# Kernel optimization log

Hardware: AMD Instinct MI355X
Metric: run time of the kernel (lower is better)

Reference implementation:

```python
import jax, jax.numpy as jnp
import numpy as np
from jax import lax

B, J, C, K, TOK, CH, H = 2048, 17, 480, 3, 64, 960, 6
HD = C // H  # 80
EPS = 1e-5

def gelu(x):
    return jax.nn.gelu(x, approximate=False)

def layernorm(x, g, b):
    mu = jnp.mean(x, axis=-1, keepdims=True)
    var = jnp.var(x, axis=-1, keepdims=True)
    return (x - mu) * lax.rsqrt(var + EPS) * g + b

def groupnorm(x, g, b, groups=16):
    # x: (B, C, J) -> normalize over (C//groups * J) per group
    n, c, j = x.shape
    xg = x.reshape(n, groups, -1)
    mu = jnp.mean(xg, axis=-1, keepdims=True)
    var = jnp.var(xg, axis=-1, keepdims=True)
    xg = (xg - mu) * lax.rsqrt(var + EPS)
    return xg.reshape(n, c, j) * g[None, :, None] + b[None, :, None]

def dwconv1d(x, w, b, pad):
    # x: (B, C, J), w: (C, 1, Kw) depthwise
    y = lax.conv_general_dilated(x, w, window_strides=(1,), padding=[(pad, pad)],
                                 dimension_numbers=('NCH', 'OIH', 'NCH'),
                                 feature_group_count=x.shape[1])
    return y + b[None, :, None]

def setup_inputs() -> dict:
    key = jax.random.key(0)
    ks = jax.random.split(key, 16)
    n = jax.random.normal
    return {
        'x': n(ks[0], (B, J, C), dtype=jnp.float32),
        'adj': n(ks[1], (K, J, J), dtype=jnp.float32) * 0.1,
        'norm1_g': jnp.ones((J,), jnp.float32), 'norm1_b': jnp.zeros((J,), jnp.float32),
        'gcn1_w': n(ks[2], (C * K, C), jnp.float32) * 0.02, 'gcn1_b': jnp.zeros((C * K,), jnp.float32),
        'dw_w': n(ks[3], (C, 1, 7), jnp.float32) * 0.1, 'dw_b': jnp.zeros((C,), jnp.float32),
        'dwgn_g': jnp.ones((C,), jnp.float32), 'dwgn_b': jnp.zeros((C,), jnp.float32),
        'mlp1_w1': n(ks[4], (TOK, J), jnp.float32) * 0.02, 'mlp1_b1': jnp.zeros((TOK,), jnp.float32),
        'mlp1_w2': n(ks[5], (J, TOK), jnp.float32) * 0.02, 'mlp1_b2': jnp.zeros((J,), jnp.float32),
        'qkv_w': n(ks[6], (3 * C, C), jnp.float32) * 0.02, 'qkv_b': jnp.zeros((3 * C,), jnp.float32),
        'proj_w': n(ks[7], (C, C), jnp.float32) * 0.02, 'proj_b': jnp.zeros((C,), jnp.float32),
        'pos_w': n(ks[8], (C, 1, 9), jnp.float32) * 0.1, 'pos_b': jnp.zeros((C,), jnp.float32),
        'gnf_g': jnp.ones((C,), jnp.float32), 'gnf_b': jnp.zeros((C,), jnp.float32),
        'norm2_g': jnp.ones((C,), jnp.float32), 'norm2_b': jnp.zeros((C,), jnp.float32),
        'gcn2_w': n(ks[9], (C * K, C), jnp.float32) * 0.02, 'gcn2_b': jnp.zeros((C * K,), jnp.float32),
        'mlp2_w1': n(ks[10], (CH, C), jnp.float32) * 0.02, 'mlp2_b1': jnp.zeros((CH,), jnp.float32),
        'mlp2_w2': n(ks[11], (C, CH), jnp.float32) * 0.02, 'mlp2_b2': jnp.zeros((C,), jnp.float32),
    }

def reference(x, adj, norm1_g, norm1_b, gcn1_w, gcn1_b, dw_w, dw_b, dwgn_g, dwgn_b,
              mlp1_w1, mlp1_b1, mlp1_w2, mlp1_b2, qkv_w, qkv_b, proj_w, proj_b,
              pos_w, pos_b, gnf_g, gnf_b, norm2_g, norm2_b, gcn2_w, gcn2_b,
              mlp2_w1, mlp2_b1, mlp2_w2, mlp2_b2):
    b = x.shape[0]
    xc = jnp.transpose(x, (0, 2, 1))            # (b, c, j)
    res_spatial = xc
    xn = layernorm(xc, norm1_g, norm1_b)        # LN over joints
    # --- GCN branch 1: 1x1 conv then adjacency einsum ---
    y = jnp.einsum('bcj,oc->boj', xn, gcn1_w) + gcn1_b[None, :, None]
    y = y.reshape(b, K, C, J)
    x_gcn1 = jnp.einsum('bkcv,kvw->bcw', y, adj)  # (b, c, j)
    # --- depthwise conv + GN + GELU + token Mlp ---
    d = gelu(groupnorm(dwconv1d(xn, dw_w, dw_b, 3), dwgn_g, dwgn_b))
    x_mjem = gelu(d @ mlp1_w1.T + mlp1_b1) @ mlp1_w2.T + mlp1_b2  # mix over j
    # --- spatial global attention (6 heads over joints + dwconv pos) ---
    xt = jnp.transpose(xn, (0, 2, 1))           # (b, j, c)
    qkv = xt @ qkv_w.T + qkv_b                  # (b, j, 3c)
    qkv = qkv.reshape(b, J, 3, H, HD).transpose(2, 0, 3, 1, 4)  # (3, b, h, j, hd)
    q, k, v = qkv[0], qkv[1], qkv[2]
    attn = jax.nn.softmax(jnp.einsum('bhqd,bhkd->bhqk', q, k) * (HD ** -0.5), axis=-1)
    o = jnp.einsum('bhqk,bhkd->bhqd', attn, v).transpose(0, 2, 1, 3).reshape(b, J, C)
    o = o @ proj_w.T + proj_b
    x_gsa = jnp.transpose(o, (0, 2, 1)) + dwconv1d(xn, pos_w, pos_b, 4)  # (b, c, j)
    # --- fuse ---
    fused = groupnorm(x_gsa + x_gcn1 + x_mjem, gnf_g, gnf_b)
    xc = res_spatial + gelu(fused)
    # --- channel stage ---
    xj = jnp.transpose(xc, (0, 2, 1))           # (b, j, c)
    res_channel = xj
    xn2 = layernorm(xj, norm2_g, norm2_b)       # LN over channels
    xcc = jnp.transpose(xn2, (0, 2, 1))         # (b, c, j)
    y2 = jnp.einsum('bcj,oc->boj', xcc, gcn2_w) + gcn2_b[None, :, None]
    y2 = y2.reshape(b, K, C, J)
    x_gcn2 = jnp.transpose(jnp.einsum('bkcv,kvw->bcw', y2, adj), (0, 2, 1))  # (b, j, c)
    mlp_out = gelu(xn2 @ mlp2_w1.T + mlp2_b1) @ mlp2_w2.T + mlp2_b2
    # sca_block is undefined in the source __init__ -> identity
    return res_channel + mlp_out + x_gcn2
```

## Files before the change

kernel.cpp:

```cpp
#include <hip/hip_runtime.h>
#include <hip/hip_bf16.h>

#define DI __device__ __forceinline__

typedef __attribute__((ext_vector_type(8))) short bf16x8;
typedef __attribute__((ext_vector_type(4))) float f32x4;

namespace {
constexpr int B_ = 2048, J_ = 17, C_ = 480, K_ = 3, TOK_ = 64, CH_ = 960, H_ = 6, HD_ = 80;
constexpr int C3_ = 3 * C_;
constexpr float EPSF = 1e-5f;
}

DI float gelu_f(float x) { return 0.5f * x * (1.0f + erff(x * 0.70710678118654752f)); }
DI float b2f(__hip_bfloat16 v) { return __bfloat162float(v); }
DI __hip_bfloat16 f2b(float v) { return __float2bfloat16(v); }
DI float s2f(short s) { return __uint_as_float(((unsigned)(unsigned short)s) << 16); }

DI void gl16(const void* g, void* l) {
  __builtin_amdgcn_global_load_lds(
      (const __attribute__((address_space(1))) unsigned int*)g,
      (__attribute__((address_space(3))) unsigned int*)l, 16, 0, 0);
}

__global__ __launch_bounds__(256) void cvt_all_kernel(
    const float* __restrict__ s0, const float* __restrict__ s1,
    const float* __restrict__ s2, const float* __restrict__ s3,
    const float* __restrict__ s4, const float* __restrict__ s5,
    __hip_bfloat16* __restrict__ d) {
  constexpr int SG = C3_ * C_;
  constexpr int O1 = SG, O2 = 2 * SG, O3 = 3 * SG;
  constexpr int O4 = O3 + C_ * C_;
  constexpr int O5 = O4 + CH_ * C_;
  const int i = (blockIdx.x * 256 + threadIdx.x) * 4;
  const float* s; int off;
  if      (i < O1) { s = s0; off = i; }
  else if (i < O2) { s = s1; off = i - O1; }
  else if (i < O3) { s = s2; off = i - O2; }
  else if (i < O4) { s = s3; off = i - O3; }
  else if (i < O5) { s = s4; off = i - O4; }
  else             { s = s5; off = i - O5; }
  const float4 v = *reinterpret_cast<const float4*>(s + off);
  union { ushort4 u; __hip_bfloat16 h[4]; } o;
  o.h[0] = f2b(v.x); o.h[1] = f2b(v.y); o.h[2] = f2b(v.z); o.h[3] = f2b(v.w);
  *reinterpret_cast<ushort4*>(reinterpret_cast<unsigned short*>(d) + i) = o.u;
}

__global__ __launch_bounds__(256) void ln1_kernel(const float* __restrict__ x,
                                                  const float* __restrict__ g,
                                                  const float* __restrict__ bt,
                                                  __hip_bfloat16* __restrict__ xnT, int nBC) {
  const int t = blockIdx.x * 256 + threadIdx.x;
  if (t >= nBC) return;
  const int b = t / C_, c = t % C_;
  const float* xp = x + (size_t)b * J_ * C_ + c;
  float v[J_];
  float s = 0.f;
  #pragma unroll
  for (int j = 0; j < J_; ++j) { v[j] = xp[j * C_]; s += v[j]; }
  const float mu = s * (1.f / J_);
  float sq = 0.f;
  #pragma unroll
  for (int j = 0; j < J_; ++j) { const float d = v[j] - mu; sq += d * d; }
  const float rs = rsqrtf(sq * (1.f / J_) + EPSF);
  __hip_bfloat16* op = xnT + (size_t)b * J_ * C_ + c;
  #pragma unroll
  for (int j = 0; j < J_; ++j) op[j * C_] = f2b((v[j] - mu) * rs * g[j] + bt[j]);
}

template<int KD, int EPI>
__global__ __launch_bounds__(256) void gemm_lds(const __hip_bfloat16* __restrict__ A,
                                                const __hip_bfloat16* __restrict__ W,
                                                const float* __restrict__ bias,
                                                __hip_bfloat16* __restrict__ Dst, int Ntot,
                                                const __hip_bfloat16* __restrict__ r1,
                                                const __hip_bfloat16* __restrict__ r2,
                                                float* __restrict__ outf) {
  constexpr int NST = (KD + 63) / 64;
  constexpr bool TAIL = (KD % 64) != 0;
  constexpr int ROWB = KD * 2;
  __shared__ __align__(16) char smem[57344];

  const int lane = threadIdx.x & 63;
  const int wid  = threadIdx.x >> 6;
  const int m0g = blockIdx.x * 128;
  const int n0g = blockIdx.y * 96;

  const int srow = lane >> 3;
  const int scbs = ((lane & 7) * 16) ^ ((srow & 7) << 4);
  auto stage = [&](int t, int bi) {
    const int kb = t * 128;
    const int ab = bi * 16384;
    const int bb = 32768 + bi * 12288;
    #pragma unroll
    for (int i = wid; i < 16; i += 4) {
      const int r = i * 8 + srow;
      gl16((const char*)A + (size_t)(m0g + r) * ROWB + kb + scbs, smem + ab + i * 1024);
    }
    #pragma unroll
    for (int i = wid; i < 12; i += 4) {
      const int r = i * 8 + srow;
      gl16((const char*)W + (size_t)(n0g + r) * ROWB + kb + scbs, smem + bb + i * 1024);
    }
  };

  const f32x4 zf = {0.f, 0.f, 0.f, 0.f};
  f32x4 acc[4][3];
  #pragma unroll
  for (int mi = 0; mi < 4; ++mi)
    #pragma unroll
    for (int ni = 0; ni < 3; ++ni) acc[mi][ni] = zf;

  const int rA0 = (wid >> 1) * 64 + (lane & 15);
  const int rB0 = (wid & 1) * 48 + (lane & 15);
  const int swz = (lane & 7) << 4;
  const int kq  = (lane >> 4) * 16;

  stage(0, 0);
  __syncthreads();
  int buf = 0;
  for (int t = 0; t < NST; ++t) {
    if (t + 1 < NST) stage(t + 1, buf ^ 1);
    const int abase = buf * 16384;
    const int bbase = 32768 + buf * 12288;
    const int nks = (TAIL && t == NST - 1) ? 1 : 2;
    for (int ks = 0; ks < nks; ++ks) {
      const int cb = (ks * 64 + kq) ^ swz;
      bf16x8 av[4], bv[3];
      #pragma unroll
      for (int mi = 0; mi < 4; ++mi)
        av[mi] = *reinterpret_cast<const bf16x8*>(smem + abase + (rA0 + mi * 16) * 128 + cb);
      #pragma unroll
      for (int ni = 0; ni < 3; ++ni)
        bv[ni] = *reinterpret_cast<const bf16x8*>(smem + bbase + (rB0 + ni * 16) * 128 + cb);
      #pragma unroll
      for (int mi = 0; mi < 4; ++mi)
        #pragma unroll
        for (int ni = 0; ni < 3; ++ni)
          acc[mi][ni] = __builtin_amdgcn_mfma_f32_16x16x32_bf16(av[mi], bv[ni], acc[mi][ni], 0, 0, 0);
    }
    __syncthreads();
    buf ^= 1;
  }

  const int col0 = n0g + (wid & 1) * 48 + (lane & 15);
  const int r0   = m0g + (wid >> 1) * 64 + ((lane >> 4) << 2);
  #pragma unroll
  for (int ni = 0; ni < 3; ++ni) {
    const int col = col0 + ni * 16;
    const float bvv = bias[col];
    #pragma unroll
    for (int mi = 0; mi < 4; ++mi) {
      #pragma unroll
      for (int r = 0; r < 4; ++r) {
        const size_t idx = (size_t)(r0 + mi * 16 + r) * Ntot + col;
        float v = acc[mi][ni][r] + bvv;
        if (EPI == 1) v = gelu_f(v);
        if (EPI == 2) outf[idx] = v + b2f(r1[idx]) + b2f(r2[idx]);
        else Dst[idx] = f2b(v);
      }
    }
  }
}

__global__ __launch_bounds__(256) void attn_kernel(const __hip_bfloat16* __restrict__ qkv,
                                                   __hip_bfloat16* __restrict__ o) {
  const int b = blockIdx.x, tid = threadIdx.x;
  __shared__ __hip_bfloat16 sqkv[J_][C3_];
  __shared__ float S[H_][J_][J_];
  {
    const uint4* src = (const uint4*)(qkv + (size_t)b * J_ * C3_);
    uint4* dst = (uint4*)&sqkv[0][0];
    for (int i = tid; i < 3060; i += 256) dst[i] = src[i];
  }
  __syncthreads();
  for (int i = tid; i < H_ * J_ * J_; i += 256) {
    const int h = i / (J_ * J_), r = i % (J_ * J_), qj = r / J_, kj = r % J_;
    const bf16x8* qp = (const bf16x8*)&sqkv[qj][h * HD_];
    const bf16x8* kp = (const bf16x8*)&sqkv[kj][C_ + h * HD_];
    float acc = 0.f;
    #pragma unroll
    for (int d8 = 0; d8 < HD_ / 8; ++d8) {
      const bf16x8 qv = qp[d8], kv = kp[d8];
      #pragma unroll
      for (int t = 0; t < 8; ++t) acc += s2f(qv[t]) * s2f(kv[t]);
    }
    S[h][qj][kj] = acc * 0.11180339887498949f;
  }
  __syncthreads();
  if (tid < H_ * J_) {
    const int h = tid / J_, qj = tid % J_;
    float* row = S[h][qj];
    float m = row[0];
    #pragma unroll
    for (int kk = 1; kk < J_; ++kk) m = fmaxf(m, row[kk]);
    float s = 0.f;
    #pragma unroll
    for (int kk = 0; kk < J_; ++kk) { const float e = __expf(row[kk] - m); row[kk] = e; s += e; }
    const float inv = 1.f / s;
    #pragma unroll
    for (int kk = 0; kk < J_; ++kk) row[kk] *= inv;
  }
  __syncthreads();
  __hip_bfloat16* ob = o + (size_t)b * J_ * C_;
  for (int i = tid; i < J_ * C_; i += 256) {
    const int qj = i / C_, c = i % C_;
    const int h = c / HD_;
    const float* srow = S[h][qj];
    float acc = 0.f;
    #pragma unroll
    for (int kk = 0; kk < J_; ++kk) acc += srow[kk] * b2f(sqkv[kk][2 * C_ + c]);
    ob[i] = f2b(acc);
  }
}

__global__ __launch_bounds__(512) void gcn_contract_kernel(const __hip_bfloat16* __restrict__ y,
                                                           const float* __restrict__ adj,
                                                           __hip_bfloat16* __restrict__ g) {
  const int b = blockIdx.x, tid = threadIdx.x;
  __shared__ float adjl[K_ * J_ * J_];
  for (int i = tid; i < K_ * J_ * J_; i += 512) adjl[i] = adj[i];
  __syncthreads();
  const int c = tid;
  if (c < C_) {
    float yv[K_][J_];
    const __hip_bfloat16* yb = y + (size_t)b * J_ * C3_ + c;
    #pragma unroll
    for (int k = 0; k < K_; ++k)
      #pragma unroll
      for (int v = 0; v < J_; ++v)
        yv[k][v] = b2f(yb[(size_t)v * C3_ + k * C_]);
    __hip_bfloat16* gp = g + (size_t)b * J_ * C_ + c;
    #pragma unroll
    for (int w = 0; w < J_; ++w) {
      float acc = 0.f;
      #pragma unroll
      for (int k = 0; k < K_; ++k)
        #pragma unroll
        for (int v = 0; v < J_; ++v)
          acc += yv[k][v] * adjl[(k * J_ + v) * J_ + w];
      gp[w * C_] = f2b(acc);
    }
  }
}

__global__ __launch_bounds__(512) void dwmlp_kernel(const __hip_bfloat16* __restrict__ xnT,
    const float* __restrict__ dww, const float* __restrict__ dwb,
    const float* __restrict__ gg, const float* __restrict__ gb,
    const float* __restrict__ w1, const float* __restrict__ b1,
    const float* __restrict__ w2, const float* __restrict__ b2,
    __hip_bfloat16* __restrict__ mjem) {
  const int b = blockIdx.x, tid = threadIdx.x;
  __shared__ __hip_bfloat16 xl[J_][C_];
  __shared__ float gstat[16][2];
  {
    const uint4* src = (const uint4*)(xnT + (size_t)b * J_ * C_);
    uint4* dst = (uint4*)&xl[0][0];
    for (int i = tid; i < 1020; i += 512) dst[i] = src[i];
  }
  if (tid < 32) gstat[tid >> 1][tid & 1] = 0.f;
  __syncthreads();
  const int c = tid;
  float dv[J_];
  if (c < C_) {
    float wv[7];
    #pragma unroll
    for (int t = 0; t < 7; ++t) wv[t] = dww[c * 7 + t];
    const float bias = dwb[c];
    float s = 0.f, sqs = 0.f;
    #pragma unroll
    for (int j = 0; j < J_; ++j) {
      float acc = bias;
      #pragma unroll
      for (int t = 0; t < 7; ++t) {
        const int jj = j - 3 + t;
        if (jj >= 0 && jj < J_) acc += b2f(xl[jj][c]) * wv[t];
      }
      dv[j] = acc; s += acc; sqs += acc * acc;
    }
    atomicAdd(&gstat[c / 30][0], s);
    atomicAdd(&gstat[c / 30][1], sqs);
  }
  __syncthreads();
  if (c < C_) {
    const float mu = gstat[c / 30][0] * (1.f / 510.f);
    const float var = gstat[c / 30][1] * (1.f / 510.f) - mu * mu;
    const float rs = rsqrtf(var + EPSF);
    const float sc = gg[c], of = gb[c];
    #pragma unroll
    for (int j = 0; j < J_; ++j) dv[j] = gelu_f((dv[j] - mu) * rs * sc + of);
    float h[TOK_];
    #pragma unroll
    for (int t = 0; t < TOK_; ++t) h[t] = b1[t];
    #pragma unroll
    for (int j = 0; j < J_; ++j) {
      const float d = dv[j];
      #pragma unroll
      for (int t = 0; t < TOK_; ++t) h[t] = fmaf(d, w1[t * J_ + j], h[t]);
    }
    #pragma unroll
    for (int t = 0; t < TOK_; ++t) h[t] = gelu_f(h[t]);
    float mj[J_];
    #pragma unroll
    for (int j = 0; j < J_; ++j) mj[j] = b2[j];
    #pragma unroll
    for (int t = 0; t < TOK_; ++t) {
      const float hg = h[t];
      #pragma unroll
      for (int j = 0; j < J_; ++j) mj[j] = fmaf(hg, w2[j * TOK_ + t], mj[j]);
    }
    __hip_bfloat16* dst = mjem + (size_t)b * J_ * C_ + c;
    #pragma unroll
    for (int j = 0; j < J_; ++j) dst[j * C_] = f2b(mj[j]);
  }
}

__global__ __launch_bounds__(512) void fuse_kernel(
    const float* __restrict__ x, const __hip_bfloat16* __restrict__ xnT,
    const __hip_bfloat16* __restrict__ g1o, const __hip_bfloat16* __restrict__ projo,
    const __hip_bfloat16* __restrict__ mjem,
    const float* __restrict__ posw, const float* __restrict__ posb,
    const float* __restrict__ gnfg, const float* __restrict__ gnfb,
    const float* __restrict__ n2g, const float* __restrict__ n2b,
    __hip_bfloat16* __restrict__ resch, __hip_bfloat16* __restrict__ xn2) {
  const int b = blockIdx.x, tid = threadIdx.x;
  __shared__ float xcl[J_][C_];
  __shared__ float gstat[16][2];
  __shared__ float lnst[J_][2];
  if (tid < 32) gstat[tid >> 1][tid & 1] = 0.f;
  __syncthreads();
  const int c = tid;
  float fz[J_];
  if (c < C_) {
    float xnv[J_];
    const __hip_bfloat16* xp = xnT + (size_t)b * J_ * C_ + c;
    #pragma unroll
    for (int j = 0; j < J_; ++j) xnv[j] = b2f(xp[j * C_]);
    float pw[9];
    #pragma unroll
    for (int t = 0; t < 9; ++t) pw[t] = posw[c * 9 + t];
    const float pb = posb[c];
    const __hip_bfloat16* pj = projo + (size_t)b * J_ * C_ + c;
    const __hip_bfloat16* mp = mjem + (size_t)b * J_ * C_ + c;
    const __hip_bfloat16* gp = g1o + (size_t)b * J_ * C_ + c;
    float s = 0.f, sqs = 0.f;
    #pragma unroll
    for (int j = 0; j < J_; ++j) {
      float pos = pb;
      #pragma unroll
      for (int t = 0; t < 9; ++t) {
        const int jj = j - 4 + t;
        if (jj >= 0 && jj < J_) pos += xnv[jj] * pw[t];
      }
      const float f = b2f(pj[j * C_]) + pos + b2f(gp[j * C_]) + b2f(mp[j * C_]);
      fz[j] = f; s += f; sqs += f * f;
    }
    atomicAdd(&gstat[c / 30][0], s);
    atomicAdd(&gstat[c / 30][1], sqs);
  }
  __syncthreads();
  if (c < C_) {
    const float mu = gstat[c / 30][0] * (1.f / 510.f);
    const float var = gstat[c / 30][1] * (1.f / 510.f) - mu * mu;
    const float rs = rsqrtf(var + EPSF);
    const float sc = gnfg[c], of = gnfb[c];
    const float* xr = x + (size_t)b * J_ * C_ + c;
    __hip_bfloat16* rp = resch + (size_t)b * J_ * C_ + c;
    #pragma unroll
    for (int j = 0; j < J_; ++j) {
      const float xcv = xr[j * C_] + gelu_f((fz[j] - mu) * rs * sc + of);
      xcl[j][c] = xcv;
      rp[j * C_] = f2b(xcv);
    }
  }
  __syncthreads();
  const int wid = tid >> 6, lane = tid & 63;
  for (int j = wid; j < J_; j += 8) {
    float ls = 0.f, lq = 0.f;
    for (int cc = lane; cc < C_; cc += 64) { const float v = xcl[j][cc]; ls += v; lq += v * v; }
    #pragma unroll
    for (int off = 32; off > 0; off >>= 1) { ls += __shfl_xor(ls, off); lq += __shfl_xor(lq, off); }
    if (lane == 0) {
      const float mu = ls * (1.f / C_);
      const float var = lq * (1.f / C_) - mu * mu;
      lnst[j][0] = mu; lnst[j][1] = rsqrtf(var + EPSF);
    }
  }
  __syncthreads();
  if (c < C_) {
    const float sc = n2g[c], of = n2b[c];
    __hip_bfloat16* xp2 = xn2 + (size_t)b * J_ * C_ + c;
    #pragma unroll
    for (int j = 0; j < J_; ++j)
      xp2[j * C_] = f2b((xcl[j][c] - lnst[j][0]) * lnst[j][1] * sc + of);
  }
}

extern "C" void kernel_launch(void* const* d_in, const int* in_sizes, int n_in,
                              void* d_out, int out_size, void* d_ws, size_t ws_size,
                              hipStream_t stream) {
  const float* x      = (const float*)d_in[0];
  const float* adj    = (const float*)d_in[1];
  const float* n1g    = (const float*)d_in[2];
  const float* n1b    = (const float*)d_in[3];
  const float* gcn1_w = (const float*)d_in[4];
  const float* gcn1_b = (const float*)d_in[5];
  const float* dw_w   = (const float*)d_in[6];
  const float* dw_b   = (const float*)d_in[7];
  const float* dwgn_g = (const float*)d_in[8];
  const float* dwgn_b = (const float*)d_in[9];
  const float* m1w1   = (const float*)d_in[10];
  const float* m1b1   = (const float*)d_in[11];
  const float* m1w2   = (const float*)d_in[12];
  const float* m1b2   = (const float*)d_in[13];
  const float* qkv_w  = (const float*)d_in[14];
  const float* qkv_b  = (const float*)d_in[15];
  const float* proj_w = (const float*)d_in[16];
  const float* proj_b = (const float*)d_in[17];
  const float* pos_w  = (const float*)d_in[18];
  const float* pos_b  = (const float*)d_in[19];
  const float* gnf_g  = (const float*)d_in[20];
  const float* gnf_b  = (const float*)d_in[21];
  const float* n2g    = (const float*)d_in[22];
  const float* n2b    = (const float*)d_in[23];
  const float* gcn2_w = (const float*)d_in[24];
  const float* gcn2_b = (const float*)d_in[25];
  const float* m2w1   = (const float*)d_in[26];
  const float* m2b1   = (const float*)d_in[27];
  const float* m2w2   = (const float*)d_in[28];
  const float* m2b2   = (const float*)d_in[29];
  float* out = (float*)d_out;
  char* ws = (char*)d_ws;
  (void)in_sizes; (void)n_in; (void)out_size;

  auto a256 = [](size_t b) { return (b + 255) & ~(size_t)255; };
  const size_t wbytes = 3 * a256((size_t)C3_ * C_ * 2) + a256((size_t)C_ * C_ * 2) +
                        a256((size_t)CH_ * C_ * 2) + a256((size_t)C_ * CH_ * 2);
  int nch = 16;
  for (int cand : {1, 2, 4, 8, 16}) {
    const size_t Mcb = (size_t)(B_ / cand) * J_;
    const size_t fp = wbytes + a256(Mcb * C3_ * 2) + 6 * a256(Mcb * C_ * 2);
    if (fp <= ws_size) { nch = cand; break; }
  }
  const int Bc = B_ / nch;
  const int Mc = Bc * J_;

  size_t off = 0;
  auto alloc = [&](size_t bytes) { char* p = ws + off; off += a256(bytes); return p; };
  __hip_bfloat16* w_qkv = (__hip_bfloat16*)alloc((size_t)C3_ * C_ * 2);
  __hip_bfloat16* w_g1  = (__hip_bfloat16*)alloc((size_t)C3_ * C_ * 2);
  __hip_bfloat16* w_g2  = (__hip_bfloat16*)alloc((size_t)C3_ * C_ * 2);
  __hip_bfloat16* w_pr  = (__hip_bfloat16*)alloc((size_t)C_ * C_ * 2);
  __hip_bfloat16* w_21  = (__hip_bfloat16*)alloc((size_t)CH_ * C_ * 2);
  __hip_bfloat16* w_22  = (__hip_bfloat16*)alloc((size_t)C_ * CH_ * 2);
  __hip_bfloat16* BIG   = (__hip_bfloat16*)alloc((size_t)Mc * C3_ * 2);
  __hip_bfloat16* xnT   = (__hip_bfloat16*)alloc((size_t)Mc * C_ * 2);
  __hip_bfloat16* attno = (__hip_bfloat16*)alloc((size_t)Mc * C_ * 2);
  __hip_bfloat16* projo = (__hip_bfloat16*)alloc((size_t)Mc * C_ * 2);
  __hip_bfloat16* mjem  = (__hip_bfloat16*)alloc((size_t)Mc * C_ * 2);
  __hip_bfloat16* g1o   = (__hip_bfloat16*)alloc((size_t)Mc * C_ * 2);
  __hip_bfloat16* resch = (__hip_bfloat16*)alloc((size_t)Mc * C_ * 2);
  __hip_bfloat16* xn2   = attno;
  __hip_bfloat16* g2o   = g1o;
  __hip_bfloat16* hbuf  = BIG;

  cvt_all_kernel<<<3150, 256, 0, stream>>>(qkv_w, gcn1_w, gcn2_w, proj_w, m2w1, m2w2, w_qkv);

  for (int ci = 0; ci < nch; ++ci) {
    const float* xc = x + (size_t)ci * Bc * J_ * C_;
    float* outc = out + (size_t)ci * Bc * J_ * C_;
    ln1_kernel<<<(Bc * C_ + 255) / 256, 256, 0, stream>>>(xc, n1g, n1b, xnT, Bc * C_);
    gemm_lds<C_, 0><<<dim3(Mc / 128, C3_ / 96), 256, 0, stream>>>(xnT, w_qkv, qkv_b, BIG, C3_, nullptr, nullptr, nullptr);
    attn_kernel<<<Bc, 256, 0, stream>>>(BIG, attno);
    gemm_lds<C_, 0><<<dim3(Mc / 128, C3_ / 96), 256, 0, stream>>>(xnT, w_g1, gcn1_b, BIG, C3_, nullptr, nullptr, nullptr);
    gcn_contract_kernel<<<Bc, 512, 0, stream>>>(BIG, adj, g1o);
    gemm_lds<C_, 0><<<dim3(Mc / 128, C_ / 96), 256, 0, stream>>>(attno, w_pr, proj_b, projo, C_, nullptr, nullptr, nullptr);
    dwmlp_kernel<<<Bc, 512, 0, stream>>>(xnT, dw_w, dw_b, dwgn_g, dwgn_b, m1w1, m1b1, m1w2, m1b2, mjem);
    fuse_kernel<<<Bc, 512, 0, stream>>>(xc, xnT, g1o, projo, mjem, pos_w, pos_b,
                                        gnf_g, gnf_b, n2g, n2b, resch, xn2);
    gemm_lds<C_, 0><<<dim3(Mc / 128, C3_ / 96), 256, 0, stream>>>(xn2, w_g2, gcn2_b, BIG, C3_, nullptr, nullptr, nullptr);
    gcn_contract_kernel<<<Bc, 512, 0, stream>>>(BIG, adj, g2o);
    gemm_lds<C_, 1><<<dim3(Mc / 128, CH_ / 96), 256, 0, stream>>>(xn2, w_21, m2b1, hbuf, CH_, nullptr, nullptr, nullptr);
    gemm_lds<CH_, 2><<<dim3(Mc / 128, C_ / 96), 256, 0, stream>>>(hbuf, w_22, m2b2, nullptr, C_, resch, g2o, outc);
  }
}
```

Measured before the change: 835.8 us.

## Run token-mixing MLP on MFMA in dwmlp kernel and use tanh-approx GELU

The per-channel scalar FMA loops of the token-mixing MLP (17->64->17) in dwmlp_kernel are replaced with bf16 MFMA 16x16x32 tiles. Weights are staged in LDS as padded bf16, and the GELU'd depthwise output is packed into LDS as the B operand. Hidden activations are written back through LDS for the second MFMA. Separately, the erf GELU used everywhere is replaced by the tanh/sigmoid approximation x/(1+exp(z)), which lowers transcendental cost but changes numerics and adds bf16 rounding of the intermediates.

```diff
diff --git a/kernel.cpp b/kernel.cpp
--- a/kernel.cpp
+++ b/kernel.cpp
@@ -12,10 +12,20 @@
 constexpr float EPSF = 1e-5f;
 }
 
-DI float gelu_f(float x) { return 0.5f * x * (1.0f + erff(x * 0.70710678118654752f)); }
+DI float gelu_f(float x) {
+  const float kA2 = 2.f * 0.7978845608028654f;
+  const float kB2 = 2.f * 0.7978845608028654f * 0.044715f;
+  const float z = fmaf(-kB2 * x, x * x, -kA2 * x);
+  return x / (1.f + __expf(z));
+}
 DI float b2f(__hip_bfloat16 v) { return __bfloat162float(v); }
 DI __hip_bfloat16 f2b(float v) { return __float2bfloat16(v); }
 DI float s2f(short s) { return __uint_as_float(((unsigned)(unsigned short)s) << 16); }
+DI unsigned pk2(float a, float b) {
+  union { unsigned u; __hip_bfloat16 h[2]; } p;
+  p.h[0] = f2b(a); p.h[1] = f2b(b);
+  return p.u;
+}
 
 DI void gl16(const void* g, void* l) {
   __builtin_amdgcn_global_load_lds(
@@ -250,19 +260,38 @@
     const float* __restrict__ w1, const float* __restrict__ b1,
     const float* __restrict__ w2, const float* __restrict__ b2,
     __hip_bfloat16* __restrict__ mjem) {
+  __shared__ __align__(16) char lds[66560];
+  __shared__ float gstat[16][2];
+  constexpr int XL = 0, DT = 18432, W1P = 56832, W2P = 61952;
   const int b = blockIdx.x, tid = threadIdx.x;
-  __shared__ __hip_bfloat16 xl[J_][C_];
-  __shared__ float gstat[16][2];
+  const int lane = tid & 63, wid = tid >> 6;
+
   {
     const uint4* src = (const uint4*)(xnT + (size_t)b * J_ * C_);
-    uint4* dst = (uint4*)&xl[0][0];
+    uint4* dst = (uint4*)(lds + XL);
     for (int i = tid; i < 1020; i += 512) dst[i] = src[i];
   }
+  {
+    __hip_bfloat16* wp = (__hip_bfloat16*)(lds + W1P);
+    for (int i = tid; i < 64 * 40; i += 512) {
+      const int t = i / 40, j = i % 40;
+      wp[i] = (j < J_) ? f2b(w1[t * J_ + j]) : f2b(0.f);
+    }
+  }
+  {
+    __hip_bfloat16* wp = (__hip_bfloat16*)(lds + W2P);
+    for (int i = tid; i < 32 * 72; i += 512) {
+      const int j = i / 72, t = i % 72;
+      wp[i] = (j < J_ && t < TOK_) ? f2b(w2[j * TOK_ + t]) : f2b(0.f);
+    }
+  }
   if (tid < 32) gstat[tid >> 1][tid & 1] = 0.f;
   __syncthreads();
+
   const int c = tid;
   float dv[J_];
   if (c < C_) {
+    const __hip_bfloat16* xl = (const __hip_bfloat16*)(lds + XL);
     float wv[7];
     #pragma unroll
     for (int t = 0; t < 7; ++t) wv[t] = dww[c * 7 + t];
@@ -274,7 +303,7 @@
       #pragma unroll
       for (int t = 0; t < 7; ++t) {
         const int jj = j - 3 + t;
-        if (jj >= 0 && jj < J_) acc += b2f(xl[jj][c]) * wv[t];
+        if (jj >= 0 && jj < J_) acc += b2f(xl[jj * C_ + c]) * wv[t];
       }
       dv[j] = acc; s += acc; sqs += acc * acc;
     }
@@ -289,29 +318,68 @@
     const float sc = gg[c], of = gb[c];
     #pragma unroll
     for (int j = 0; j < J_; ++j) dv[j] = gelu_f((dv[j] - mu) * rs * sc + of);
-    float h[TOK_];
-    #pragma unroll
-    for (int t = 0; t < TOK_; ++t) h[t] = b1[t];
-    #pragma unroll
-    for (int j = 0; j < J_; ++j) {
-      const float d = dv[j];
-      #pragma unroll
-      for (int t = 0; t < TOK_; ++t) h[t] = fmaf(d, w1[t * J_ + j], h[t]);
-    }
-    #pragma unroll
-    for (int t = 0; t < TOK_; ++t) h[t] = gelu_f(h[t]);
-    float mj[J_];
-    #pragma unroll
-    for (int j = 0; j < J_; ++j) mj[j] = b2[j];
-    #pragma unroll
-    for (int t = 0; t < TOK_; ++t) {
-      const float hg = h[t];
-      #pragma unroll
-      for (int j = 0; j < J_; ++j) mj[j] = fmaf(hg, w2[j * TOK_ + t], mj[j]);
-    }
-    __hip_bfloat16* dst = mjem + (size_t)b * J_ * C_ + c;
-    #pragma unroll
-    for (int j = 0; j < J_; ++j) dst[j * C_] = f2b(mj[j]);
+    unsigned* rp = (unsigned*)(lds + DT + c * 80);
+    #pragma unroll
+    for (int p = 0; p < 8; ++p) rp[p] = pk2(dv[2 * p], dv[2 * p + 1]);
+    rp[8] = pk2(dv[16], 0.f);
+    #pragma unroll
+    for (int p = 9; p < 16; ++p) rp[p] = 0u;
+  }
+  __syncthreads();
+
+  const int lr = lane & 15, kc = lane >> 4;
+  bf16x8 a1[4];
+  #pragma unroll
+  for (int mi = 0; mi < 4; ++mi)
+    a1[mi] = *(const bf16x8*)(lds + W1P + (lr + mi * 16) * 80 + kc * 16);
+  bf16x8 a2[2][2];
+  #pragma unroll
+  for (int mi = 0; mi < 2; ++mi)
+    #pragma unroll
+    for (int kk = 0; kk < 2; ++kk)
+      a2[mi][kk] = *(const bf16x8*)(lds + W2P + (lr + mi * 16) * 144 + kk * 64 + kc * 16);
+  float b1v[4][4];
+  #pragma unroll
+  for (int mi = 0; mi < 4; ++mi)
+    #pragma unroll
+    for (int r = 0; r < 4; ++r) b1v[mi][r] = b1[mi * 16 + kc * 4 + r];
+  float b2v[4];
+  #pragma unroll
+  for (int r = 0; r < 4; ++r) b2v[r] = b2[kc * 4 + r];
+  const float b2v16 = b2[16];
+
+  char* hs = lds + XL + wid * 2304;
+  const f32x4 zf4 = {0.f, 0.f, 0.f, 0.f};
+  for (int cb = wid; cb < 30; cb += 8) {
+    const int c0 = cb * 16;
+    const bf16x8 bf = *(const bf16x8*)(lds + DT + (c0 + lr) * 80 + kc * 16);
+    f32x4 acc1[4];
+    #pragma unroll
+    for (int mi = 0; mi < 4; ++mi)
+      acc1[mi] = __builtin_amdgcn_mfma_f32_16x16x32_bf16(a1[mi], bf, zf4, 0, 0, 0);
+    #pragma unroll
+    for (int mi = 0; mi < 4; ++mi) {
+      const float g0 = gelu_f(acc1[mi][0] + b1v[mi][0]);
+      const float g1 = gelu_f(acc1[mi][1] + b1v[mi][1]);
+      const float g2 = gelu_f(acc1[mi][2] + b1v[mi][2]);
+      const float g3 = gelu_f(acc1[mi][3] + b1v[mi][3]);
+      unsigned* hp = (unsigned*)(hs + lr * 144 + (mi * 16 + kc * 4) * 2);
+      hp[0] = pk2(g0, g1);
+      hp[1] = pk2(g2, g3);
+    }
+    f32x4 acc2[2] = {zf4, zf4};
+    #pragma unroll
+    for (int kk = 0; kk < 2; ++kk) {
+      const bf16x8 hb = *(const bf16x8*)(hs + lr * 144 + kk * 64 + kc * 16);
+      #pragma unroll
+      for (int mi = 0; mi < 2; ++mi)
+        acc2[mi] = __builtin_amdgcn_mfma_f32_16x16x32_bf16(a2[mi][kk], hb, acc2[mi], 0, 0, 0);
+    }
+    __hip_bfloat16* mp = mjem + (size_t)b * J_ * C_ + (c0 + lr);
+    #pragma unroll
+    for (int r = 0; r < 4; ++r)
+      mp[(kc * 4 + r) * C_] = f2b(acc2[0][r] + b2v[r]);
+    if (kc == 0) mp[16 * C_] = f2b(acc2[1][0] + b2v16);
   }
 }
 
```

New measurement: 738.4 us. 11.6% less time.
